# Kernel tuning notes

Measured on AMD Instinct MI355X. Metric: run time of the kernel, lower is better.

Reference implementation:

```python
import jax, jax.numpy as jnp
import numpy as np

D = 10       # window length (days)
STRIDE = 10  # window stride


def setup_inputs() -> dict:
    key = jax.random.key(0)
    X = jax.random.normal(key, (16384, 15, 100), dtype=jnp.float32)
    return {"X": X}


def reference(X):
    # X: [B, n, T]
    B, n, T = X.shape
    w = (T - D) // STRIDE + 1
    # Gather all windows at once: [B, n, w, D]
    idx = jnp.arange(w)[:, None] * STRIDE + jnp.arange(D)[None, :]  # [w, D]
    win = X[:, :, idx]  # [B, n, w, D]

    mean = jnp.mean(win, axis=-1, keepdims=True)
    c = win - mean                                  # centered, [B, n, w, D]
    # torch.std is unbiased (ddof=1)
    std = jnp.sqrt(jnp.sum(c * c, axis=-1) / (D - 1))  # [B, n, w]

    # Population covariance between all channel pairs via one batched Gram matmul
    gram = jnp.einsum('biwd,bjwd->bijw', c, c) / D   # [B, n, n, w]

    # Pair order in the original: j=0..n-2 paired with k=j+1..n-1 == row-major upper triangle
    ii, jj = jnp.triu_indices(n, k=1)
    cov = gram[:, ii, jj]                            # [B, h, w]
    corr = cov / (std[:, ii] * std[:, jj])           # [B, h, w]
    return corr
```

## Files before the change

### kernel.cpp

```cpp
#include <hip/hip_runtime.h>


#define NB    16384
#define NSER  15
#define TLEN  100
#define DWIN  10
#define WCNT  10
#define NPAIR 105

__global__ __launch_bounds__(64, 3) void ts_corr_kernel(const float* __restrict__ X,
                                                        float* __restrict__ out) {
    const int task = blockIdx.x * 64 + threadIdx.x;
    const int b = task / WCNT;
    const int w = task % WCNT;

    const float* Xb = X + (size_t)b * (NSER * TLEN) + w * DWIN;

    float win[NSER][DWIN];
    #pragma unroll
    for (int i = 0; i < NSER; ++i) {
        const float2* p2 = reinterpret_cast<const float2*>(Xb + i * TLEN);
        #pragma unroll
        for (int k = 0; k < 5; ++k) {
            float2 v = p2[k];
            win[i][2 * k]     = v.x;
            win[i][2 * k + 1] = v.y;
        }
    }

    float istd[NSER];
    #pragma unroll
    for (int i = 0; i < NSER; ++i) {
        float s = 0.f;
        #pragma unroll
        for (int d = 0; d < DWIN; ++d) s += win[i][d];
        const float m = s * (1.0f / DWIN);
        float sq = 0.f;
        #pragma unroll
        for (int d = 0; d < DWIN; ++d) {
            const float c = win[i][d] - m;
            win[i][d] = c;
            sq += c * c;
        }
        istd[i] = rsqrtf(sq * (1.0f / (DWIN - 1)));
    }

    float* o = out + (size_t)b * (NPAIR * WCNT) + w;
    int p = 0;
    #pragma unroll
    for (int i = 0; i < NSER; ++i) {
        #pragma unroll
        for (int j = i + 1; j < NSER; ++j) {
            float dot = 0.f;
            #pragma unroll
            for (int d = 0; d < DWIN; ++d) dot += win[i][d] * win[j][d];
            o[(size_t)p * WCNT] = dot * (1.0f / DWIN) * istd[i] * istd[j];
            ++p;
        }
    }
}

extern "C" void kernel_launch(void* const* d_in, const int* in_sizes, int n_in,
                              void* d_out, int out_size, void* d_ws, size_t ws_size,
                              hipStream_t stream) {
    const float* X = (const float*)d_in[0];
    float* out = (float*)d_out;
    const int total = NB * WCNT;
    const int block = 64;
    const int grid = (total + block - 1) / block;
    ts_corr_kernel<<<grid, block, 0, stream>>>(X, out);
}
```

Baseline: 188.9 us.

## Tile series into groups of three to cut register use, raise block size

Each thread now keeps only two groups of three series in registers instead of all fifteen windows. It walks the group pairs and reloads groups from global memory, which should be cached, to cover every pair block. Statistics use raw sums, with covariance computed as dot/D - mu_i*mu_j, so the data is never centered. Blocks grow from 64 to 256 threads with no min-occupancy hint. The intent is lower VGPR pressure and higher occupancy, paid for with repeated global loads and the numerical risk of the one-pass variance formula.

Result: faster. 182.3 us (-3.5%).

```diff
diff --git a/kernel.cpp b/kernel.cpp
--- a/kernel.cpp
+++ b/kernel.cpp
@@ -1,63 +1,96 @@
 #include <hip/hip_runtime.h>
 
 
-#define NB    16384
-#define NSER  15
-#define TLEN  100
-#define DWIN  10
-#define WCNT  10
-#define NPAIR 105
+#define NSER   15
+#define TLEN   100
+#define DWIN   10
+#define WCNT   10
+#define NPAIR  105
 
-__global__ __launch_bounds__(64, 3) void ts_corr_kernel(const float* __restrict__ X,
-                                                        float* __restrict__ out) {
-    const int task = blockIdx.x * 64 + threadIdx.x;
+template <int G>
+__device__ inline void load3(const float* __restrict__ Xb, float R[3][DWIN]) {
+    #pragma unroll
+    for (int r = 0; r < 3; ++r) {
+        const float2* p2 = reinterpret_cast<const float2*>(Xb + (G * 3 + r) * TLEN);
+        #pragma unroll
+        for (int k = 0; k < 5; ++k) {
+            float2 v = p2[k];
+            R[r][2 * k] = v.x; R[r][2 * k + 1] = v.y;
+        }
+    }
+}
+
+template <int G>
+__device__ inline void stats3(const float R[3][DWIN], float* mu, float* isd) {
+    #pragma unroll
+    for (int r = 0; r < 3; ++r) {
+        float s1 = 0.f, s2 = 0.f;
+        #pragma unroll
+        for (int d = 0; d < DWIN; ++d) { s1 += R[r][d]; s2 += R[r][d] * R[r][d]; }
+        const float m = s1 * 0.1f;
+        mu[G * 3 + r]  = m;
+        isd[G * 3 + r] = rsqrtf((s2 - 10.f * m * m) * (1.f / 9.f));
+    }
+}
+
+__device__ inline void emit(float* __restrict__ ob, int i, int j, float dot,
+                            const float* mu, const float* isd) {
+    const int p = i * (29 - i) / 2 + (j - i - 1);
+    ob[p * WCNT] = (dot * 0.1f - mu[i] * mu[j]) * isd[i] * isd[j];
+}
+
+template <int GA, int GB>
+__device__ inline void rect(const float A[3][DWIN], const float B[3][DWIN],
+                            const float* mu, const float* isd, float* __restrict__ ob) {
+    #pragma unroll
+    for (int ri = 0; ri < 3; ++ri) {
+        #pragma unroll
+        for (int rj = 0; rj < 3; ++rj) {
+            float dot = 0.f;
+            #pragma unroll
+            for (int d = 0; d < DWIN; ++d) dot += A[ri][d] * B[rj][d];
+            emit(ob, GA * 3 + ri, GB * 3 + rj, dot, mu, isd);
+        }
+    }
+}
+
+template <int G>
+__device__ inline void tri(const float A[3][DWIN],
+                           const float* mu, const float* isd, float* __restrict__ ob) {
+    #pragma unroll
+    for (int ri = 0; ri < 3; ++ri) {
+        #pragma unroll
+        for (int rj = ri + 1; rj < 3; ++rj) {
+            float dot = 0.f;
+            #pragma unroll
+            for (int d = 0; d < DWIN; ++d) dot += A[ri][d] * A[rj][d];
+            emit(ob, G * 3 + ri, G * 3 + rj, dot, mu, isd);
+        }
+    }
+}
+
+__global__ __launch_bounds__(256) void ts_corr_kernel(const float* __restrict__ X,
+                                                      float* __restrict__ out) {
+    const int task = blockIdx.x * 256 + threadIdx.x;
     const int b = task / WCNT;
     const int w = task % WCNT;
 
     const float* Xb = X + (size_t)b * (NSER * TLEN) + w * DWIN;
+    float* ob = out + (size_t)b * (NPAIR * WCNT) + w;
 
-    float win[NSER][DWIN];
-    #pragma unroll
-    for (int i = 0; i < NSER; ++i) {
-        const float2* p2 = reinterpret_cast<const float2*>(Xb + i * TLEN);
-        #pragma unroll
-        for (int k = 0; k < 5; ++k) {
-            float2 v = p2[k];
-            win[i][2 * k]     = v.x;
-            win[i][2 * k + 1] = v.y;
-        }
-    }
+    float S[3][DWIN], T[3][DWIN], mu[NSER], isd[NSER];
 
-    float istd[NSER];
-    #pragma unroll
-    for (int i = 0; i < NSER; ++i) {
-        float s = 0.f;
-        #pragma unroll
-        for (int d = 0; d < DWIN; ++d) s += win[i][d];
-        const float m = s * (1.0f / DWIN);
-        float sq = 0.f;
-        #pragma unroll
-        for (int d = 0; d < DWIN; ++d) {
-            const float c = win[i][d] - m;
-            win[i][d] = c;
-            sq += c * c;
-        }
-        istd[i] = rsqrtf(sq * (1.0f / (DWIN - 1)));
-    }
-
-    float* o = out + (size_t)b * (NPAIR * WCNT) + w;
-    int p = 0;
-    #pragma unroll
-    for (int i = 0; i < NSER; ++i) {
-        #pragma unroll
-        for (int j = i + 1; j < NSER; ++j) {
-            float dot = 0.f;
-            #pragma unroll
-            for (int d = 0; d < DWIN; ++d) dot += win[i][d] * win[j][d];
-            o[(size_t)p * WCNT] = dot * (1.0f / DWIN) * istd[i] * istd[j];
-            ++p;
-        }
-    }
+    load3<0>(Xb, S); stats3<0>(S, mu, isd); tri<0>(S, mu, isd, ob);
+    load3<1>(Xb, T); stats3<1>(T, mu, isd); rect<0,1>(S, T, mu, isd, ob); tri<1>(T, mu, isd, ob);
+    load3<2>(Xb, S); stats3<2>(S, mu, isd); rect<1,2>(T, S, mu, isd, ob); tri<2>(S, mu, isd, ob);
+    load3<3>(Xb, T); stats3<3>(T, mu, isd); rect<2,3>(S, T, mu, isd, ob); tri<3>(T, mu, isd, ob);
+    load3<4>(Xb, S); stats3<4>(S, mu, isd); rect<3,4>(T, S, mu, isd, ob); tri<4>(S, mu, isd, ob);
+    load3<0>(Xb, T); rect<0,4>(T, S, mu, isd, ob);
+    load3<2>(Xb, S); rect<0,2>(T, S, mu, isd, ob);
+    load3<4>(Xb, T); rect<2,4>(S, T, mu, isd, ob);
+    load3<1>(Xb, S); rect<1,4>(S, T, mu, isd, ob);
+    load3<3>(Xb, T); rect<1,3>(S, T, mu, isd, ob);
+    load3<0>(Xb, S); rect<0,3>(S, T, mu, isd, ob);
 }
 
 extern "C" void kernel_launch(void* const* d_in, const int* in_sizes, int n_in,
@@ -65,8 +98,6 @@
                               hipStream_t stream) {
     const float* X = (const float*)d_in[0];
     float* out = (float*)d_out;
-    const int total = NB * WCNT;
-    const int block = 64;
-    const int grid = (total + block - 1) / block;
-    ts_corr_kernel<<<grid, block, 0, stream>>>(X, out);
+    const int total = 16384 * WCNT;
+    ts_corr_kernel<<<total / 256, 256, 0, stream>>>(X, out);
 }
```
